# Performance work log

Measured on AMD Instinct MI355X. Metric: run time of the kernel, lower is better.

The kernel has to match this reference:

```python
import jax, jax.numpy as jnp
import numpy as np

B, S, D = 16, 4096, 128
LN_EPS = 1e-5
REC_EPS = 1e-8


def setup_inputs() -> dict:
    key = jax.random.key(0)
    k1, k2, k3, k4 = jax.random.split(key, 4)
    return {
        "C": jax.random.normal(k1, (B, S, D), dtype=jnp.float32),
        "V": jax.random.normal(k2, (B, S, D), dtype=jnp.float32),
        "W": jax.random.normal(k3, (B, S, D), dtype=jnp.float32),
        "encoder_context": jax.random.normal(k4, (B, D), dtype=jnp.float32),
        "time_modulation": jnp.full((1, 1, D), 0.5, dtype=jnp.float32),
        "context_modulation": jnp.full((1, D), 0.5, dtype=jnp.float32),
        "ln_weight": jnp.ones((D,), dtype=jnp.float32),
        "ln_bias": jnp.zeros((D,), dtype=jnp.float32),
    }


def reference(C, V, W, encoder_context, time_modulation, context_modulation, ln_weight, ln_bias):
    b_, s_, d_ = C.shape
    tm = time_modulation[0, 0]  # [D]
    # context gate is time-invariant: compute once
    ctx_add = jax.nn.sigmoid(encoder_context * context_modulation) * encoder_context  # [B,D]

    def step(carry, xs):
        a, bst = carry  # a: [B,1], bst: [B,D]
        c_t, v_t, w_t = xs  # each [B,D]
        decay = jax.nn.sigmoid(w_t * tm)  # [B,D]
        ec = jnp.exp(c_t)  # [B,D]
        a = decay.mean(axis=1, keepdims=True) * a + ec.sum(axis=1, keepdims=True)
        bst = decay * bst + ec * v_t + ctx_add
        out_t = bst / (a + REC_EPS)
        return (a, bst), out_t

    a0 = jnp.zeros((b_, 1), dtype=C.dtype)
    b0 = jnp.zeros((b_, d_), dtype=C.dtype)
    xs = (jnp.swapaxes(C, 0, 1), jnp.swapaxes(V, 0, 1), jnp.swapaxes(W, 0, 1))  # [S,B,D]
    _, ys = jax.lax.scan(step, (a0, b0), xs)  # ys: [S,B,D]
    res = jnp.swapaxes(ys, 0, 1)  # [B,S,D]

    mu = jnp.mean(res, axis=-1, keepdims=True)
    var = jnp.var(res, axis=-1, keepdims=True)
    normed = (res - mu) * jax.lax.rsqrt(var + LN_EPS)
    return normed * ln_weight + ln_bias
```

## Files before the change

kernel.cpp:

```cpp
#include <hip/hip_runtime.h>

#define BB   16
#define SS   4096
#define DD   128
#define NCH  256
#define TT   (SS / NCH)
#define WPB  4
#define NTHR 256

#define DT   16
#define SUBS 16
#define CPS  (NCH / SUBS)

#define LN_EPS  1e-5f
#define REC_EPS 1e-8f

__device__ __forceinline__ float fast_rcp(float x) { return __builtin_amdgcn_rcpf(x); }
__device__ __forceinline__ float sigm(float x) { return fast_rcp(1.0f + __expf(-x)); }

__device__ __forceinline__ unsigned pack_de(float d, float e) {
    unsigned ud = (__float_as_uint(d) + 0x8000u) >> 16;
    unsigned ue = (__float_as_uint(e) + 0x8000u) & 0xFFFF0000u;
    return ue | ud;
}
__device__ __forceinline__ float de_lo(unsigned u) { return __uint_as_float(u << 16); }
__device__ __forceinline__ float de_hi(unsigned u) { return __uint_as_float(u & 0xFFFF0000u); }

template<int CTRL>
__device__ __forceinline__ float dpp_mov0(float x) {
    return __int_as_float(
        __builtin_amdgcn_update_dpp(0, __float_as_int(x), CTRL, 0xF, 0xF, true));
}

__device__ __forceinline__ void wave_red2(float& a, float& b) {
    a += dpp_mov0<0x111>(a); b += dpp_mov0<0x111>(b);
    a += dpp_mov0<0x112>(a); b += dpp_mov0<0x112>(b);
    a += dpp_mov0<0x114>(a); b += dpp_mov0<0x114>(b);
    a += dpp_mov0<0x118>(a); b += dpp_mov0<0x118>(b);
    a += dpp_mov0<0x142>(a); b += dpp_mov0<0x142>(b);
    a += dpp_mov0<0x143>(a); b += dpp_mov0<0x143>(b);
    a = __int_as_float(__builtin_amdgcn_readlane(__float_as_int(a), 63));
    b = __int_as_float(__builtin_amdgcn_readlane(__float_as_int(b), 63));
}

__global__ __launch_bounds__(NTHR, 2) void pass1_kernel(
    const float* __restrict__ C, const float* __restrict__ V, const float* __restrict__ W,
    const float* __restrict__ enc, const float* __restrict__ tmod, const float* __restrict__ cmod,
    unsigned* __restrict__ DE,
    float* __restrict__ Pbuf, float* __restrict__ Qbuf,
    float* __restrict__ PaBuf, float* __restrict__ QaBuf,
    float2* __restrict__ MEbuf)
{
    const int wv   = threadIdx.x >> 6;
    const int lane = threadIdx.x & 63;
    const int gc   = blockIdx.x * WPB + wv;
    const int b    = gc >> 8;
    const int ch   = gc & (NCH - 1);
    const int d2   = lane << 1;

    const int t0 = ch * TT;
    const size_t base = ((size_t)b * SS + t0) * DD + d2;
    const float2* Cp = (const float2*)(C + base);
    const float2* Vp = (const float2*)(V + base);
    const float2* Wp = (const float2*)(W + base);
    uint2* DEp = (uint2*)(DE + base);

    float2 cR[TT], wR[TT], vR[TT];
#pragma unroll
    for (int t = 0; t < TT; ++t) cR[t] = Cp[t * (DD / 2)];
#pragma unroll
    for (int t = 0; t < TT; ++t) wR[t] = Wp[t * (DD / 2)];
#pragma unroll
    for (int t = 0; t < TT; ++t) vR[t] = Vp[t * (DD / 2)];

    const float2 tm = *(const float2*)(tmod + d2);
    const float2 cm = *(const float2*)(cmod + d2);
    const float2 ec = *(const float2*)(enc + b * DD + d2);
    float2 ctx;
    ctx.x = sigm(ec.x * cm.x) * ec.x;
    ctx.y = sigm(ec.y * cm.y) * ec.y;

    float2 P = make_float2(1.f, 1.f);
    float2 Q = make_float2(0.f, 0.f);
    float pa = 1.f, qa = 0.f;
    float mkeep = 0.f, ekeep = 0.f;

#pragma unroll
    for (int t = 0; t < TT; ++t) {
        float2 dec, e2;
        dec.x = sigm(wR[t].x * tm.x); dec.y = sigm(wR[t].y * tm.y);
        e2.x = __expf(cR[t].x); e2.y = __expf(cR[t].y);

        uint2 u;
        u.x = pack_de(dec.x, e2.x); u.y = pack_de(dec.y, e2.y);
        DEp[t * (DD / 2)] = u;

        Q.x = dec.x * Q.x + (e2.x * vR[t].x + ctx.x);
        Q.y = dec.y * Q.y + (e2.y * vR[t].y + ctx.y);
        P.x *= dec.x; P.y *= dec.y;

        float sd = dec.x + dec.y;
        float se = e2.x + e2.y;
        wave_red2(sd, se);
        const float mt = sd * (1.0f / DD);
        pa *= mt;
        qa = mt * qa + se;
        if (lane == t) { mkeep = mt; ekeep = se; }
    }

    *(float2*)(Pbuf + (size_t)gc * DD + d2) = P;
    *(float2*)(Qbuf + (size_t)gc * DD + d2) = Q;
    if (lane < TT) MEbuf[(size_t)b * SS + t0 + lane] = make_float2(mkeep, ekeep);
    if (lane == 0) { PaBuf[gc] = pa; QaBuf[gc] = qa; }
}

__global__ __launch_bounds__(256) void pass2_kernel(
    const float* __restrict__ Pbuf, const float* __restrict__ Qbuf,
    const float* __restrict__ PaBuf, const float* __restrict__ QaBuf,
    float* __restrict__ bst0, float* __restrict__ a0)
{
    const int b   = blockIdx.x >> 3;
    const int dt  = blockIdx.x & 7;
    const int tid = threadIdx.x;
    const int dl  = tid & (DT - 1);
    const int sub = tid >> 4;
    const int d   = dt * DT + dl;

    __shared__ float cP[SUBS][DT], cQ[SUBS][DT], ent[SUBS][DT];
    __shared__ float sPa[NCH], sQa[NCH];

    const int ch0 = sub * CPS;
    const size_t base = ((size_t)b * NCH + ch0) * DD + d;
    float Pr[CPS], Qr[CPS];
    float p = 1.f, q = 0.f;
#pragma unroll
    for (int i = 0; i < CPS; ++i) {
        Pr[i] = Pbuf[base + (size_t)i * DD];
        Qr[i] = Qbuf[base + (size_t)i * DD];
        q = Pr[i] * q + Qr[i];
        p = Pr[i] * p;
    }
    cP[sub][dl] = p; cQ[sub][dl] = q;
    __syncthreads();

    if (tid < DT) {
        float s = 0.f;
#pragma unroll
        for (int sb = 0; sb < SUBS; ++sb) {
            ent[sb][tid] = s;
            s = cP[sb][tid] * s + cQ[sb][tid];
        }
    }
    __syncthreads();

    float s = ent[sub][dl];
#pragma unroll
    for (int i = 0; i < CPS; ++i) {
        bst0[base + (size_t)i * DD] = s;
        s = Pr[i] * s + Qr[i];
    }

    if (dt == 0) {
        float pa = PaBuf[b * NCH + tid];
        float qa = QaBuf[b * NCH + tid];
#pragma unroll
        for (int off = 1; off < NCH; off <<= 1) {
            sPa[tid] = pa; sQa[tid] = qa;
            __syncthreads();
            if (tid >= off) {
                const float pp = sPa[tid - off], qq = sQa[tid - off];
                qa = pa * qq + qa;
                pa = pa * pp;
            }
            __syncthreads();
        }
        sQa[tid] = qa;
        __syncthreads();
        a0[b * NCH + tid] = (tid == 0) ? 0.f : sQa[tid - 1];
    }
}

__global__ __launch_bounds__(NTHR, 2) void pass3_kernel(
    const float* __restrict__ V, const unsigned* __restrict__ DE,
    const float* __restrict__ enc, const float* __restrict__ cmod,
    const float* __restrict__ lnw, const float* __restrict__ lnb,
    const float* __restrict__ bst0, const float* __restrict__ a0,
    const float2* __restrict__ MEbuf,
    float* __restrict__ out)
{
    const int wv   = threadIdx.x >> 6;
    const int lane = threadIdx.x & 63;
    const int gc   = blockIdx.x * WPB + wv;
    const int b    = gc >> 8;
    const int ch   = gc & (NCH - 1);
    const int d2   = lane << 1;

    const int t0 = ch * TT;
    const size_t base = ((size_t)b * SS + t0) * DD + d2;
    const float2* Vp  = (const float2*)(V + base);
    const uint2*  DEp = (const uint2*)(DE + base);
    float2* Op = (float2*)(out + base);

    float2 vR[TT]; uint2 deR[TT];
#pragma unroll
    for (int t = 0; t < TT; ++t) deR[t] = DEp[t * (DD / 2)];
#pragma unroll
    for (int t = 0; t < TT; ++t) vR[t] = Vp[t * (DD / 2)];
    const float2 me = MEbuf[(size_t)b * SS + t0 + (lane & (TT - 1))];

    const float2 cm = *(const float2*)(cmod + d2);
    const float2 ec = *(const float2*)(enc + b * DD + d2);
    float2 ctx;
    ctx.x = sigm(ec.x * cm.x) * ec.x;
    ctx.y = sigm(ec.y * cm.y) * ec.y;
    const float2 gw = *(const float2*)(lnw + d2);
    const float2 gb = *(const float2*)(lnb + d2);

    float2 bst = *(const float2*)(bst0 + (size_t)gc * DD + d2);
    float a = a0[gc];

#pragma unroll
    for (int t = 0; t < TT; ++t) {
        const float mt = __int_as_float(__builtin_amdgcn_readlane(__float_as_int(me.x), t));
        const float et = __int_as_float(__builtin_amdgcn_readlane(__float_as_int(me.y), t));

        a = mt * a + et;
        bst.x = de_lo(deR[t].x) * bst.x + (de_hi(deR[t].x) * vR[t].x + ctx.x);
        bst.y = de_lo(deR[t].y) * bst.y + (de_hi(deR[t].y) * vR[t].y + ctx.y);

        const float inva = fast_rcp(a + REC_EPS);
        float2 o;
        o.x = bst.x * inva; o.y = bst.y * inva;

        float s1 = o.x + o.y;
        float s2 = o.x * o.x + o.y * o.y;
        wave_red2(s1, s2);
        const float mu  = s1 * (1.0f / DD);
        const float var = s2 * (1.0f / DD) - mu * mu;
        const float rs  = rsqrtf(var + LN_EPS);

        float2 r;
        r.x = (o.x - mu) * rs * gw.x + gb.x;
        r.y = (o.y - mu) * rs * gw.y + gb.y;
        Op[t * (DD / 2)] = r;
    }
}

extern "C" void kernel_launch(void* const* d_in, const int* in_sizes, int n_in,
                              void* d_out, int out_size, void* d_ws, size_t ws_size,
                              hipStream_t stream)
{
    const float* C    = (const float*)d_in[0];
    const float* V    = (const float*)d_in[1];
    const float* W    = (const float*)d_in[2];
    const float* enc  = (const float*)d_in[3];
    const float* tmod = (const float*)d_in[4];
    const float* cmod = (const float*)d_in[5];
    const float* lnw  = (const float*)d_in[6];
    const float* lnb  = (const float*)d_in[7];
    float* out = (float*)d_out;

    float* ws    = (float*)d_ws;
    unsigned* DEbuf = (unsigned*)ws;
    float* Pbuf  = ws    + (size_t)BB * SS * DD;
    float* Qbuf  = Pbuf  + (size_t)BB * NCH * DD;
    float* bst0  = Qbuf  + (size_t)BB * NCH * DD;
    float2* MEbuf = (float2*)(bst0 + (size_t)BB * NCH * DD);
    float* PaBuf = (float*)(MEbuf + (size_t)BB * SS);
    float* QaBuf = PaBuf + (size_t)BB * NCH;
    float* a0Buf = QaBuf + (size_t)BB * NCH;

    const int nblk = BB * NCH / WPB;
    pass1_kernel<<<nblk, NTHR, 0, stream>>>(C, V, W, enc, tmod, cmod, DEbuf,
                                            Pbuf, Qbuf, PaBuf, QaBuf, MEbuf);
    pass2_kernel<<<BB * 8, 256, 0, stream>>>(Pbuf, Qbuf, PaBuf, QaBuf, bst0, a0Buf);
    pass3_kernel<<<nblk, NTHR, 0, stream>>>(V, DEbuf, enc, cmod, lnw, lnb,
                                            bst0, a0Buf, MEbuf, out);
}
```

Measured before the change: 161.2 us.

## Store packed decay and input term so pass3 skips rereading V

New measurement: 158.9 us. Within noise of the previous version (-1.4%).

```diff
diff --git a/kernel.cpp b/kernel.cpp
--- a/kernel.cpp
+++ b/kernel.cpp
@@ -18,13 +18,13 @@
 __device__ __forceinline__ float fast_rcp(float x) { return __builtin_amdgcn_rcpf(x); }
 __device__ __forceinline__ float sigm(float x) { return fast_rcp(1.0f + __expf(-x)); }
 
-__device__ __forceinline__ unsigned pack_de(float d, float e) {
-    unsigned ud = (__float_as_uint(d) + 0x8000u) >> 16;
-    unsigned ue = (__float_as_uint(e) + 0x8000u) & 0xFFFF0000u;
-    return ue | ud;
-}
-__device__ __forceinline__ float de_lo(unsigned u) { return __uint_as_float(u << 16); }
-__device__ __forceinline__ float de_hi(unsigned u) { return __uint_as_float(u & 0xFFFF0000u); }
+__device__ __forceinline__ unsigned pack2(float a, float b) {
+    unsigned ua = (__float_as_uint(a) + 0x8000u) >> 16;
+    unsigned ub = (__float_as_uint(b) + 0x8000u) & 0xFFFF0000u;
+    return ub | ua;
+}
+__device__ __forceinline__ float up_lo(unsigned u) { return __uint_as_float(u << 16); }
+__device__ __forceinline__ float up_hi(unsigned u) { return __uint_as_float(u & 0xFFFF0000u); }
 
 template<int CTRL>
 __device__ __forceinline__ float dpp_mov0(float x) {
@@ -43,10 +43,12 @@
     b = __int_as_float(__builtin_amdgcn_readlane(__float_as_int(b), 63));
 }
 
+#define LOAD_FENCE() asm volatile("" ::: "memory")
+
 __global__ __launch_bounds__(NTHR, 2) void pass1_kernel(
     const float* __restrict__ C, const float* __restrict__ V, const float* __restrict__ W,
     const float* __restrict__ enc, const float* __restrict__ tmod, const float* __restrict__ cmod,
-    unsigned* __restrict__ DE,
+    unsigned* __restrict__ DTb,
     float* __restrict__ Pbuf, float* __restrict__ Qbuf,
     float* __restrict__ PaBuf, float* __restrict__ QaBuf,
     float2* __restrict__ MEbuf)
@@ -63,19 +65,21 @@
     const float2* Cp = (const float2*)(C + base);
     const float2* Vp = (const float2*)(V + base);
     const float2* Wp = (const float2*)(W + base);
-    uint2* DEp = (uint2*)(DE + base);
-
-    float2 cR[TT], wR[TT], vR[TT];
-#pragma unroll
-    for (int t = 0; t < TT; ++t) cR[t] = Cp[t * (DD / 2)];
-#pragma unroll
-    for (int t = 0; t < TT; ++t) wR[t] = Wp[t * (DD / 2)];
-#pragma unroll
-    for (int t = 0; t < TT; ++t) vR[t] = Vp[t * (DD / 2)];
+    uint2* DTp = (uint2*)(DTb + base);
 
     const float2 tm = *(const float2*)(tmod + d2);
     const float2 cm = *(const float2*)(cmod + d2);
     const float2 ec = *(const float2*)(enc + b * DD + d2);
+
+    float2 cR[TT], wR[TT], vR[TT];
+#pragma unroll
+    for (int t = 0; t < TT; ++t) {
+        cR[t] = Cp[t * (DD / 2)];
+        wR[t] = Wp[t * (DD / 2)];
+        vR[t] = Vp[t * (DD / 2)];
+    }
+    LOAD_FENCE();
+
     float2 ctx;
     ctx.x = sigm(ec.x * cm.x) * ec.x;
     ctx.y = sigm(ec.y * cm.y) * ec.y;
@@ -87,17 +91,21 @@
 
 #pragma unroll
     for (int t = 0; t < TT; ++t) {
-        float2 dec, e2;
+        float2 dec, e2, T2;
         dec.x = sigm(wR[t].x * tm.x); dec.y = sigm(wR[t].y * tm.y);
         e2.x = __expf(cR[t].x); e2.y = __expf(cR[t].y);
+        T2.x = e2.x * vR[t].x + ctx.x;
+        T2.y = e2.y * vR[t].y + ctx.y;
 
         uint2 u;
-        u.x = pack_de(dec.x, e2.x); u.y = pack_de(dec.y, e2.y);
-        DEp[t * (DD / 2)] = u;
-
-        Q.x = dec.x * Q.x + (e2.x * vR[t].x + ctx.x);
-        Q.y = dec.y * Q.y + (e2.y * vR[t].y + ctx.y);
-        P.x *= dec.x; P.y *= dec.y;
+        u.x = pack2(dec.x, T2.x); u.y = pack2(dec.y, T2.y);
+        DTp[t * (DD / 2)] = u;
+
+        const float dqx = up_lo(u.x), dqy = up_lo(u.y);
+        const float tqx = up_hi(u.x), tqy = up_hi(u.y);
+        Q.x = dqx * Q.x + tqx;
+        Q.y = dqy * Q.y + tqy;
+        P.x *= dqx; P.y *= dqy;
 
         float sd = dec.x + dec.y;
         float se = e2.x + e2.y;
@@ -180,9 +188,8 @@
     }
 }
 
-__global__ __launch_bounds__(NTHR, 2) void pass3_kernel(
-    const float* __restrict__ V, const unsigned* __restrict__ DE,
-    const float* __restrict__ enc, const float* __restrict__ cmod,
+__global__ __launch_bounds__(NTHR, 4) void pass3_kernel(
+    const unsigned* __restrict__ DTb,
     const float* __restrict__ lnw, const float* __restrict__ lnb,
     const float* __restrict__ bst0, const float* __restrict__ a0,
     const float2* __restrict__ MEbuf,
@@ -197,27 +204,20 @@
 
     const int t0 = ch * TT;
     const size_t base = ((size_t)b * SS + t0) * DD + d2;
-    const float2* Vp  = (const float2*)(V + base);
-    const uint2*  DEp = (const uint2*)(DE + base);
+    const uint2* DTp = (const uint2*)(DTb + base);
     float2* Op = (float2*)(out + base);
 
-    float2 vR[TT]; uint2 deR[TT];
-#pragma unroll
-    for (int t = 0; t < TT; ++t) deR[t] = DEp[t * (DD / 2)];
-#pragma unroll
-    for (int t = 0; t < TT; ++t) vR[t] = Vp[t * (DD / 2)];
+    uint2 dtR[TT];
+#pragma unroll
+    for (int t = 0; t < TT; ++t) dtR[t] = DTp[t * (DD / 2)];
     const float2 me = MEbuf[(size_t)b * SS + t0 + (lane & (TT - 1))];
-
-    const float2 cm = *(const float2*)(cmod + d2);
-    const float2 ec = *(const float2*)(enc + b * DD + d2);
-    float2 ctx;
-    ctx.x = sigm(ec.x * cm.x) * ec.x;
-    ctx.y = sigm(ec.y * cm.y) * ec.y;
+    float2 bst = *(const float2*)(bst0 + (size_t)gc * DD + d2);
+    const float a_in = a0[gc];
     const float2 gw = *(const float2*)(lnw + d2);
     const float2 gb = *(const float2*)(lnb + d2);
-
-    float2 bst = *(const float2*)(bst0 + (size_t)gc * DD + d2);
-    float a = a0[gc];
+    LOAD_FENCE();
+
+    float a = a_in;
 
 #pragma unroll
     for (int t = 0; t < TT; ++t) {
@@ -225,8 +225,8 @@
         const float et = __int_as_float(__builtin_amdgcn_readlane(__float_as_int(me.y), t));
 
         a = mt * a + et;
-        bst.x = de_lo(deR[t].x) * bst.x + (de_hi(deR[t].x) * vR[t].x + ctx.x);
-        bst.y = de_lo(deR[t].y) * bst.y + (de_hi(deR[t].y) * vR[t].y + ctx.y);
+        bst.x = up_lo(dtR[t].x) * bst.x + up_hi(dtR[t].x);
+        bst.y = up_lo(dtR[t].y) * bst.y + up_hi(dtR[t].y);
 
         const float inva = fast_rcp(a + REC_EPS);
         float2 o;
@@ -261,7 +261,7 @@
     float* out = (float*)d_out;
 
     float* ws    = (float*)d_ws;
-    unsigned* DEbuf = (unsigned*)ws;
+    unsigned* DTbuf = (unsigned*)ws;
     float* Pbuf  = ws    + (size_t)BB * SS * DD;
     float* Qbuf  = Pbuf  + (size_t)BB * NCH * DD;
     float* bst0  = Qbuf  + (size_t)BB * NCH * DD;
@@ -271,9 +271,9 @@
     float* a0Buf = QaBuf + (size_t)BB * NCH;
 
     const int nblk = BB * NCH / WPB;
-    pass1_kernel<<<nblk, NTHR, 0, stream>>>(C, V, W, enc, tmod, cmod, DEbuf,
+    pass1_kernel<<<nblk, NTHR, 0, stream>>>(C, V, W, enc, tmod, cmod, DTbuf,
                                             Pbuf, Qbuf, PaBuf, QaBuf, MEbuf);
     pass2_kernel<<<BB * 8, 256, 0, stream>>>(Pbuf, Qbuf, PaBuf, QaBuf, bst0, a0Buf);
-    pass3_kernel<<<nblk, NTHR, 0, stream>>>(V, DEbuf, enc, cmod, lnw, lnb,
+    pass3_kernel<<<nblk, NTHR, 0, stream>>>(DTbuf, lnw, lnb,
                                             bst0, a0Buf, MEbuf, out);
 }
```
